# Optimization experiments

Hardware: AMD Instinct MI355X
Metric: run time of the kernel (lower is better)

Reference implementation:

```python
import jax, jax.numpy as jnp
import numpy as np
from jax import lax

NJ = 14
COL = 14
SIGMA = 1.0
RADIUS = 4  # scipy gaussian_filter: truncate=4.0 * sigma=1.0 -> radius 4


def _gauss_kernel():
    x = np.arange(-RADIUS, RADIUS + 1, dtype=np.float32)
    w = np.exp(-0.5 * x * x / (SIGMA * SIGMA))
    w /= w.sum()
    return jnp.asarray(w)


def _blur(delta):
    # separable gaussian with scipy mode='reflect' (== np.pad 'symmetric')
    B, J, H, W = delta.shape
    w = _gauss_kernel()
    p = jnp.pad(delta, ((0, 0), (0, 0), (RADIUS, RADIUS), (RADIUS, RADIUS)), mode='symmetric')
    lhs = p.reshape(B * J, 1, H + 2 * RADIUS, W + 2 * RADIUS)
    kh = w.reshape(1, 1, 2 * RADIUS + 1, 1)
    kw = w.reshape(1, 1, 1, 2 * RADIUS + 1)
    dn = ('NCHW', 'OIHW', 'NCHW')
    y = lax.conv_general_dilated(lhs, kh, (1, 1), 'VALID', dimension_numbers=dn)
    y = lax.conv_general_dilated(y, kw, (1, 1), 'VALID', dimension_numbers=dn)
    return y.reshape(B, J, H, W)


def setup_inputs() -> dict:
    key = jax.random.key(0)
    k1, k2, k3, k4 = jax.random.split(key, 4)
    B = 8192
    o = jax.random.normal(k1, (B, 2 * NJ, COL, COL), jnp.float32)
    h = jax.random.uniform(k2, (B, NJ, COL, COL), jnp.float32)
    t = jax.random.uniform(k3, (B, NJ, 2), jnp.float32)
    vis = jax.random.randint(k4, (B, NJ), 0, 2).astype(jnp.float32)
    v = jnp.repeat(vis[..., None], 2, axis=-1)  # visibility duplicated over (x,y)
    return {"o": o, "h": h, "t": t, "v": v}


def reference(o, h, t, v):
    B = h.shape[0]
    scale = 1.0 / float(COL)
    f32 = jnp.float32

    # argmax coordinate extraction from predicted heatmaps
    argmax = jnp.argmax(h.reshape(B, NJ, COL * COL), axis=-1)  # [B,Nj]
    yC = argmax // COL
    xC = argmax - yC * COL
    bidx = jnp.arange(B)[:, None]
    jidx = jnp.arange(NJ)[None, :]

    h_peak = h[bidx, jidx, yC, xC]                 # [B,Nj]
    cond = h_peak > 0.5
    ox = o[bidx, jidx, yC, xC]                     # offset channels 0..Nj-1
    oy = o[bidx, jidx + NJ, yC, xC]                # offset channels Nj..2Nj-1
    x0 = jnp.where(cond, (ox + xC.astype(f32)) * scale, 0.0)
    x1 = jnp.where(cond, (oy + yC.astype(f32)) * scale, 0.0)
    x = jnp.stack([x0, x1], axis=-1)               # [B,Nj,2]

    # per-joint gaussian target heatmap (only where visible)
    ti = t * COL
    xi = jnp.clip(ti[..., 0].astype(jnp.int32), 0, COL - 1)
    yi = jnp.clip(ti[..., 1].astype(jnp.int32), 0, COL - 1)
    visf = (v[..., 0].astype(jnp.int32) == 1).astype(f32)  # [B,Nj]
    delta = jnp.zeros((B, NJ, COL, COL), f32).at[bidx, jidx, yi, xi].set(visf)
    g = _blur(delta)
    mn = g.min(axis=(-2, -1), keepdims=True)
    mx = g.max(axis=(-2, -1), keepdims=True)
    denom = jnp.where(mx > mn, mx - mn, 1.0)
    tt = jnp.where(visf[..., None, None] > 0, (g - mn) / denom, 0.0)

    # heatmap loss; original zeroes only ROW 0 of diff for invisible joints
    diff1 = h - tt
    row0 = diff1[:, :, 0:1, :] * visf[:, :, None, None]
    diff1 = jnp.concatenate([row0, diff1[:, :, 1:, :]], axis=2)
    N1 = v.sum() / 2.0
    d1 = jnp.sum(diff1 * diff1) / N1

    # coordinate loss
    diff2 = (x - t) * v
    d2 = jnp.sum(diff2 * diff2) / N1  # N2 == N1 in the original
    return d1 + d2
```

## Files before the change

kernel.cpp:

```cpp
#include <hip/hip_runtime.h>

#define NJ    14
#define TILE  196
#define BLK   256
#define JPB   64
#define STAGE_DW (JPB * TILE)

typedef __attribute__((address_space(1))) const void g_void;
typedef __attribute__((address_space(3))) void lds_void;

__device__ __forceinline__ float gtap(int d) {
  const int d2 = d * d;
  const float e = exp2f(-0.72134752044448169f * (float)d2);
  return (d2 <= 16) ? e : 0.0f;
}

__device__ __forceinline__ float uresp(int p, int pk) {
  float s = gtap(p - pk);
  if (p <= 3)  s += gtap(p + pk + 1);
  if (p >= 10) s += gtap(27 - p - pk);
  return s;
}

__device__ __forceinline__ float wave_sum(float x) {
#pragma unroll
  for (int off = 32; off >= 1; off >>= 1) x += __shfl_xor(x, off);
  return x;
}

template<int K>
__device__ __forceinline__ void accum_part(const float4* __restrict__ hp,
    const float (&uy)[14], const float (&ux)[14],
    float& bm, int& bi, float& sh2, float& cross, float& q0)
{
  const int NI = (K == 0) ? 13 : 12;
#pragma unroll
  for (int i = 0; i < NI; ++i) {
    const int f = 4 * i + K;
    const float4 q = hp[f];
    const float qa[4] = {q.x, q.y, q.z, q.w};
#pragma unroll
    for (int c = 0; c < 4; ++c) {
      const int idx = 4 * f + c;
      const int y = idx / 14;
      const int x = idx - 14 * y;
      const float hv = qa[c];
      if (hv > bm) { bm = hv; bi = idx; }
      sh2 = fmaf(hv, hv, sh2);
      if (y == 0) q0 = fmaf(hv, hv, q0);
      cross = fmaf(hv, uy[y] * ux[x], cross);
    }
  }
}

__global__ __launch_bounds__(BLK, 3) void joint_kernel(
    const float* __restrict__ o, const float* __restrict__ h,
    const float* __restrict__ t, const float* __restrict__ v,
    float* __restrict__ part, int njoint, int nblocks)
{
  __shared__ __align__(16) float lds[STAGE_DW];

  const int tid  = threadIdx.x;
  const int lane = tid & 63;
  const int wid  = tid >> 6;
  const int jg   = blockIdx.x * JPB + lane;
  const bool valid = jg < njoint;

  const int ntile = min(JPB, njoint - blockIdx.x * JPB);
  const int n4 = ntile * 49;
  const float* gbase = h + (size_t)blockIdx.x * JPB * TILE;
#pragma unroll
  for (int i = 0; i < 13; ++i) {
    const int idx = i * BLK + tid;
    if (idx < n4) {
      __builtin_amdgcn_global_load_lds(
          (g_void*)(gbase + (size_t)idx * 4),
          (lds_void*)&lds[idx * 4],
          16, 0, 0);
    }
  }

  float uy[14], ux[14];
  float2 tv = make_float2(0.0f, 0.0f);
  int xi = 0, yi = 0;
  if (valid) {
    tv = ((const float2*)t)[jg];
    xi = min(max((int)(tv.x * 14.0f), 0), 13);
    yi = min(max((int)(tv.y * 14.0f), 0), 13);
#pragma unroll
    for (int p = 0; p < 14; ++p) { uy[p] = uresp(p, yi); ux[p] = uresp(p, xi); }
  }

  asm volatile("s_waitcnt vmcnt(0)" ::: "memory");
  __syncthreads();

  float bm = -3.0e38f; int bi = 0;
  float sh2 = 0.0f, cross = 0.0f, q0 = 0.0f;
  if (valid) {
    const float4* hp = (const float4*)&lds[lane * TILE];
    switch (wid) {
      case 0: accum_part<0>(hp, uy, ux, bm, bi, sh2, cross, q0); break;
      case 1: accum_part<1>(hp, uy, ux, bm, bi, sh2, cross, q0); break;
      case 2: accum_part<2>(hp, uy, ux, bm, bi, sh2, cross, q0); break;
      default: accum_part<3>(hp, uy, ux, bm, bi, sh2, cross, q0); break;
    }
  }

  __syncthreads();
  float* red = lds;
  red[0 * BLK + tid] = bm;
  ((int*)lds)[1 * BLK + tid] = bi;
  red[2 * BLK + tid] = sh2;
  red[3 * BLK + tid] = cross;
  red[4 * BLK + tid] = q0;
  __syncthreads();

  if (wid == 0) {
    float Bm = red[lane]; int Bi = ((int*)lds)[BLK + lane];
    float S2 = red[2 * BLK + lane], Cr = red[3 * BLK + lane], Q0 = red[4 * BLK + lane];
#pragma unroll
    for (int w = 1; w < 4; ++w) {
      const float m = red[w * 64 + lane];
      const int   i = ((int*)lds)[BLK + w * 64 + lane];
      if (m > Bm || (m == Bm && i < Bi)) { Bm = m; Bi = i; }
      S2 += red[2 * BLK + w * 64 + lane];
      Cr += red[3 * BLK + w * 64 + lane];
      Q0 += red[4 * BLK + w * 64 + lane];
    }

    float s_acc = 0.0f, n_acc = 0.0f;
    if (valid) {
      const float2 vv = ((const float2*)v)[jg];
      const bool vis = ((int)vv.x) == 1;

      float Sy2 = 0.0f, Sx2 = 0.0f;
#pragma unroll
      for (int p = 0; p < 14; ++p) {
        Sy2 = fmaf(uy[p], uy[p], Sy2);
        Sx2 = fmaf(ux[p], ux[p], Sx2);
      }
      const float maxy = 1.0f + gtap(2 * yi + 1) + gtap(27 - 2 * yi);
      const float maxx = 1.0f + gtap(2 * xi + 1) + gtap(27 - 2 * xi);
      const float inv = vis ? (1.0f / (maxy * maxx)) : 0.0f;

      float s = S2 - 2.0f * inv * Cr + inv * inv * Sy2 * Sx2;
      if (!vis) s -= Q0;

      const int b = jg / NJ;
      const int j = jg - b * NJ;
      const int yC = Bi / 14;
      const int xC = Bi - 14 * yC;
      const size_t ob = ((size_t)b * (2 * NJ) + j) * TILE + (size_t)Bi;
      const float ox = o[ob];
      const float oy = o[ob + (size_t)NJ * TILE];
      const bool cond = Bm > 0.5f;
      const float sc = 1.0f / 14.0f;
      const float px = cond ? (ox + (float)xC) * sc : 0.0f;
      const float py = cond ? (oy + (float)yC) * sc : 0.0f;
      const float d0 = (px - tv.x) * vv.x;
      const float d1 = (py - tv.y) * vv.y;
      s += d0 * d0 + d1 * d1;

      s_acc = s;
      n_acc = vv.x + vv.y;
    }

    s_acc = wave_sum(s_acc);
    n_acc = wave_sum(n_acc);
    if (lane == 0) {
      part[blockIdx.x]           = s_acc;
      part[nblocks + blockIdx.x] = n_acc;
    }
  }
}

__global__ __launch_bounds__(BLK) void finalize_kernel(
    const float* __restrict__ part, float* __restrict__ out, int nblocks)
{
  float s = 0.0f, n = 0.0f;
  for (int i = threadIdx.x; i < nblocks; i += BLK) {
    s += part[i];
    n += part[nblocks + i];
  }
  s = wave_sum(s);
  n = wave_sum(n);
  __shared__ float rs[4], rn[4];
  const int lane = threadIdx.x & 63, wid = threadIdx.x >> 6;
  if (lane == 0) { rs[wid] = s; rn[wid] = n; }
  __syncthreads();
  if (threadIdx.x == 0) {
    const float S = rs[0] + rs[1] + rs[2] + rs[3];
    const float N = rn[0] + rn[1] + rn[2] + rn[3];
    out[0] = S / (0.5f * N);
  }
}

extern "C" void kernel_launch(void* const* d_in, const int* in_sizes, int n_in,
                              void* d_out, int out_size, void* d_ws, size_t ws_size,
                              hipStream_t stream)
{
  const float* o = (const float*)d_in[0];
  const float* h = (const float*)d_in[1];
  const float* t = (const float*)d_in[2];
  const float* v = (const float*)d_in[3];
  const int njoint = in_sizes[1] / TILE;
  const int nblocks = (njoint + JPB - 1) / JPB;

  float* part = (float*)d_ws;
  joint_kernel<<<nblocks, BLK, 0, stream>>>(o, h, t, v, part, njoint, nblocks);
  finalize_kernel<<<1, BLK, 0, stream>>>(part, (float*)d_out, nblocks);
}
```

Baseline: 29.91 us.

## Assign joints per wavefront and reduce quarter-tiles with lane shuffles

Each wavefront now stages its own 16 joints into a private LDS region, so the block-wide barrier after the async loads is removed. Four adjacent lanes split one joint's tile and combine their partial max, argmax and sums with xor shuffles instead of an LDS reduction handled by wave 0. The epilogue math now runs in a quarter of the lanes of every wave rather than all lanes of one wave, and only the final per-block sum still goes through LDS. Lanes sharing a joint each compute the full blur response tables, which duplicates some setup work, and the LDS reads of the four neighbouring lanes may land in a different bank pattern.

```diff
diff --git a/kernel.cpp b/kernel.cpp
--- a/kernel.cpp
+++ b/kernel.cpp
@@ -4,7 +4,8 @@
 #define TILE  196
 #define BLK   256
 #define JPB   64
-#define STAGE_DW (JPB * TILE)
+#define TPW   16
+#define REG4  (TPW * 49)
 
 typedef __attribute__((address_space(1))) const void g_void;
 typedef __attribute__((address_space(3))) void lds_void;
@@ -28,15 +29,15 @@
   return x;
 }
 
-template<int K>
+template<int Q>
 __device__ __forceinline__ void accum_part(const float4* __restrict__ hp,
     const float (&uy)[14], const float (&ux)[14],
     float& bm, int& bi, float& sh2, float& cross, float& q0)
 {
-  const int NI = (K == 0) ? 13 : 12;
+  const int NI = (Q == 0) ? 13 : 12;
 #pragma unroll
   for (int i = 0; i < NI; ++i) {
-    const int f = 4 * i + K;
+    const int f = 4 * i + Q;
     const float4 q = hp[f];
     const float qa[4] = {q.x, q.y, q.z, q.w};
 #pragma unroll
@@ -58,25 +59,29 @@
     const float* __restrict__ t, const float* __restrict__ v,
     float* __restrict__ part, int njoint, int nblocks)
 {
-  __shared__ __align__(16) float lds[STAGE_DW];
+  __shared__ __align__(16) float lds[4 * REG4 * 4];
+  __shared__ float rs[4], rn[4];
 
   const int tid  = threadIdx.x;
   const int lane = tid & 63;
   const int wid  = tid >> 6;
-  const int jg   = blockIdx.x * JPB + lane;
+  const int tl   = lane >> 2;
+  const int qq   = lane & 3;
+  const int jg   = blockIdx.x * JPB + wid * TPW + tl;
   const bool valid = jg < njoint;
 
-  const int ntile = min(JPB, njoint - blockIdx.x * JPB);
-  const int n4 = ntile * 49;
-  const float* gbase = h + (size_t)blockIdx.x * JPB * TILE;
-#pragma unroll
-  for (int i = 0; i < 13; ++i) {
-    const int idx = i * BLK + tid;
-    if (idx < n4) {
-      __builtin_amdgcn_global_load_lds(
-          (g_void*)(gbase + (size_t)idx * 4),
-          (lds_void*)&lds[idx * 4],
-          16, 0, 0);
+  {
+    const float* gsrc = h + ((size_t)blockIdx.x * JPB + wid * TPW) * TILE;
+    float* ldst = lds + (size_t)wid * REG4 * 4;
+#pragma unroll
+    for (int i = 0; i < 13; ++i) {
+      const int f4 = i * 64 + lane;
+      if (f4 < REG4) {
+        __builtin_amdgcn_global_load_lds(
+            (g_void*)(gsrc + (size_t)f4 * 4),
+            (lds_void*)(ldst + (size_t)f4 * 4),
+            16, 0, 0);
+      }
     }
   }
 
@@ -92,13 +97,12 @@
   }
 
   asm volatile("s_waitcnt vmcnt(0)" ::: "memory");
-  __syncthreads();
 
   float bm = -3.0e38f; int bi = 0;
   float sh2 = 0.0f, cross = 0.0f, q0 = 0.0f;
   if (valid) {
-    const float4* hp = (const float4*)&lds[lane * TILE];
-    switch (wid) {
+    const float4* hp = (const float4*)(lds + ((size_t)wid * REG4 + tl * 49) * 4);
+    switch (qq) {
       case 0: accum_part<0>(hp, uy, ux, bm, bi, sh2, cross, q0); break;
       case 1: accum_part<1>(hp, uy, ux, bm, bi, sh2, cross, q0); break;
       case 2: accum_part<2>(hp, uy, ux, bm, bi, sh2, cross, q0); break;
@@ -106,71 +110,60 @@
     }
   }
 
+#pragma unroll
+  for (int off = 1; off <= 2; off <<= 1) {
+    const float om = __shfl_xor(bm, off);
+    const int   oi = __shfl_xor(bi, off);
+    if (om > bm || (om == bm && oi < bi)) { bm = om; bi = oi; }
+    sh2   += __shfl_xor(sh2, off);
+    cross += __shfl_xor(cross, off);
+    q0    += __shfl_xor(q0, off);
+  }
+
+  float s_acc = 0.0f, n_acc = 0.0f;
+  if (valid && qq == 0) {
+    const float2 vv = ((const float2*)v)[jg];
+    const bool vis = ((int)vv.x) == 1;
+
+    float Sy2 = 0.0f, Sx2 = 0.0f;
+#pragma unroll
+    for (int p = 0; p < 14; ++p) {
+      Sy2 = fmaf(uy[p], uy[p], Sy2);
+      Sx2 = fmaf(ux[p], ux[p], Sx2);
+    }
+    const float maxy = 1.0f + gtap(2 * yi + 1) + gtap(27 - 2 * yi);
+    const float maxx = 1.0f + gtap(2 * xi + 1) + gtap(27 - 2 * xi);
+    const float inv = vis ? (1.0f / (maxy * maxx)) : 0.0f;
+
+    float s = sh2 - 2.0f * inv * cross + inv * inv * Sy2 * Sx2;
+    if (!vis) s -= q0;
+
+    const int b = jg / NJ;
+    const int j = jg - b * NJ;
+    const int yC = bi / 14;
+    const int xC = bi - 14 * yC;
+    const size_t ob = ((size_t)b * (2 * NJ) + j) * TILE + (size_t)bi;
+    const float ox = o[ob];
+    const float oy = o[ob + (size_t)NJ * TILE];
+    const bool cond = bm > 0.5f;
+    const float sc = 1.0f / 14.0f;
+    const float px = cond ? (ox + (float)xC) * sc : 0.0f;
+    const float py = cond ? (oy + (float)yC) * sc : 0.0f;
+    const float d0 = (px - tv.x) * vv.x;
+    const float d1 = (py - tv.y) * vv.y;
+    s += d0 * d0 + d1 * d1;
+
+    s_acc = s;
+    n_acc = vv.x + vv.y;
+  }
+
+  s_acc = wave_sum(s_acc);
+  n_acc = wave_sum(n_acc);
+  if (lane == 0) { rs[wid] = s_acc; rn[wid] = n_acc; }
   __syncthreads();
-  float* red = lds;
-  red[0 * BLK + tid] = bm;
-  ((int*)lds)[1 * BLK + tid] = bi;
-  red[2 * BLK + tid] = sh2;
-  red[3 * BLK + tid] = cross;
-  red[4 * BLK + tid] = q0;
-  __syncthreads();
-
-  if (wid == 0) {
-    float Bm = red[lane]; int Bi = ((int*)lds)[BLK + lane];
-    float S2 = red[2 * BLK + lane], Cr = red[3 * BLK + lane], Q0 = red[4 * BLK + lane];
-#pragma unroll
-    for (int w = 1; w < 4; ++w) {
-      const float m = red[w * 64 + lane];
-      const int   i = ((int*)lds)[BLK + w * 64 + lane];
-      if (m > Bm || (m == Bm && i < Bi)) { Bm = m; Bi = i; }
-      S2 += red[2 * BLK + w * 64 + lane];
-      Cr += red[3 * BLK + w * 64 + lane];
-      Q0 += red[4 * BLK + w * 64 + lane];
-    }
-
-    float s_acc = 0.0f, n_acc = 0.0f;
-    if (valid) {
-      const float2 vv = ((const float2*)v)[jg];
-      const bool vis = ((int)vv.x) == 1;
-
-      float Sy2 = 0.0f, Sx2 = 0.0f;
-#pragma unroll
-      for (int p = 0; p < 14; ++p) {
-        Sy2 = fmaf(uy[p], uy[p], Sy2);
-        Sx2 = fmaf(ux[p], ux[p], Sx2);
-      }
-      const float maxy = 1.0f + gtap(2 * yi + 1) + gtap(27 - 2 * yi);
-      const float maxx = 1.0f + gtap(2 * xi + 1) + gtap(27 - 2 * xi);
-      const float inv = vis ? (1.0f / (maxy * maxx)) : 0.0f;
-
-      float s = S2 - 2.0f * inv * Cr + inv * inv * Sy2 * Sx2;
-      if (!vis) s -= Q0;
-
-      const int b = jg / NJ;
-      const int j = jg - b * NJ;
-      const int yC = Bi / 14;
-      const int xC = Bi - 14 * yC;
-      const size_t ob = ((size_t)b * (2 * NJ) + j) * TILE + (size_t)Bi;
-      const float ox = o[ob];
-      const float oy = o[ob + (size_t)NJ * TILE];
-      const bool cond = Bm > 0.5f;
-      const float sc = 1.0f / 14.0f;
-      const float px = cond ? (ox + (float)xC) * sc : 0.0f;
-      const float py = cond ? (oy + (float)yC) * sc : 0.0f;
-      const float d0 = (px - tv.x) * vv.x;
-      const float d1 = (py - tv.y) * vv.y;
-      s += d0 * d0 + d1 * d1;
-
-      s_acc = s;
-      n_acc = vv.x + vv.y;
-    }
-
-    s_acc = wave_sum(s_acc);
-    n_acc = wave_sum(n_acc);
-    if (lane == 0) {
-      part[blockIdx.x]           = s_acc;
-      part[nblocks + blockIdx.x] = n_acc;
-    }
+  if (tid == 0) {
+    part[blockIdx.x]           = rs[0] + rs[1] + rs[2] + rs[3];
+    part[nblocks + blockIdx.x] = rn[0] + rn[1] + rn[2] + rn[3];
   }
 }
 
```

Result: slower. 39.12 us (+30.8%).

## Halve joints per block and split each joint across eight half-wave parts

Applied to the files above, without the earlier changes.

Each block now handles 32 joints instead of 64. Each wave's two halves process different float4 slices of the same joint, so work is split eight ways and combined first with a cross-half shuffle, then through LDS. The smaller LDS footprint allows a higher occupancy hint, and the finalize kernel uses 1024 threads to sum the doubled number of partials. Bounds checks are removed, which assumes the joint count is a multiple of 32.

```diff
diff --git a/kernel.cpp b/kernel.cpp
--- a/kernel.cpp
+++ b/kernel.cpp
@@ -3,8 +3,8 @@
 #define NJ    14
 #define TILE  196
 #define BLK   256
-#define JPB   64
-#define STAGE_DW (JPB * TILE)
+#define JPB   32
+#define N4    (JPB * 49)
 
 typedef __attribute__((address_space(1))) const void g_void;
 typedef __attribute__((address_space(3))) void lds_void;
@@ -28,15 +28,15 @@
   return x;
 }
 
-template<int K>
+template<int P>
 __device__ __forceinline__ void accum_part(const float4* __restrict__ hp,
     const float (&uy)[14], const float (&ux)[14],
     float& bm, int& bi, float& sh2, float& cross, float& q0)
 {
-  const int NI = (K == 0) ? 13 : 12;
+  const int NI = (P == 0) ? 7 : 6;
 #pragma unroll
   for (int i = 0; i < NI; ++i) {
-    const int f = 4 * i + K;
+    const int f = 8 * i + P;
     const float4 q = hp[f];
     const float qa[4] = {q.x, q.y, q.z, q.w};
 #pragma unroll
@@ -53,26 +53,24 @@
   }
 }
 
-__global__ __launch_bounds__(BLK, 3) void joint_kernel(
+__global__ __launch_bounds__(BLK, 6) void joint_kernel(
     const float* __restrict__ o, const float* __restrict__ h,
     const float* __restrict__ t, const float* __restrict__ v,
     float* __restrict__ part, int njoint, int nblocks)
 {
-  __shared__ __align__(16) float lds[STAGE_DW];
+  __shared__ __align__(16) float lds[N4 * 4];
 
   const int tid  = threadIdx.x;
   const int lane = tid & 63;
   const int wid  = tid >> 6;
-  const int jg   = blockIdx.x * JPB + lane;
-  const bool valid = jg < njoint;
-
-  const int ntile = min(JPB, njoint - blockIdx.x * JPB);
-  const int n4 = ntile * 49;
+  const int tl   = tid & 31;
+  const int jg   = blockIdx.x * JPB + tl;
+
   const float* gbase = h + (size_t)blockIdx.x * JPB * TILE;
 #pragma unroll
-  for (int i = 0; i < 13; ++i) {
+  for (int i = 0; i < 7; ++i) {
     const int idx = i * BLK + tid;
-    if (idx < n4) {
+    if (idx < N4) {
       __builtin_amdgcn_global_load_lds(
           (g_void*)(gbase + (size_t)idx * 4),
           (lds_void*)&lds[idx * 4],
@@ -81,55 +79,68 @@
   }
 
   float uy[14], ux[14];
-  float2 tv = make_float2(0.0f, 0.0f);
-  int xi = 0, yi = 0;
-  if (valid) {
-    tv = ((const float2*)t)[jg];
-    xi = min(max((int)(tv.x * 14.0f), 0), 13);
-    yi = min(max((int)(tv.y * 14.0f), 0), 13);
-#pragma unroll
-    for (int p = 0; p < 14; ++p) { uy[p] = uresp(p, yi); ux[p] = uresp(p, xi); }
-  }
+  const float2 tv = ((const float2*)t)[jg];
+  const int xi = min(max((int)(tv.x * 14.0f), 0), 13);
+  const int yi = min(max((int)(tv.y * 14.0f), 0), 13);
+#pragma unroll
+  for (int p = 0; p < 14; ++p) { uy[p] = uresp(p, yi); ux[p] = uresp(p, xi); }
 
   asm volatile("s_waitcnt vmcnt(0)" ::: "memory");
   __syncthreads();
 
   float bm = -3.0e38f; int bi = 0;
   float sh2 = 0.0f, cross = 0.0f, q0 = 0.0f;
-  if (valid) {
-    const float4* hp = (const float4*)&lds[lane * TILE];
+  {
+    const float4* hp = (const float4*)&lds[tl * TILE];
     switch (wid) {
-      case 0: accum_part<0>(hp, uy, ux, bm, bi, sh2, cross, q0); break;
-      case 1: accum_part<1>(hp, uy, ux, bm, bi, sh2, cross, q0); break;
-      case 2: accum_part<2>(hp, uy, ux, bm, bi, sh2, cross, q0); break;
-      default: accum_part<3>(hp, uy, ux, bm, bi, sh2, cross, q0); break;
-    }
-  }
-
-  __syncthreads();
-  float* red = lds;
-  red[0 * BLK + tid] = bm;
-  ((int*)lds)[1 * BLK + tid] = bi;
-  red[2 * BLK + tid] = sh2;
-  red[3 * BLK + tid] = cross;
-  red[4 * BLK + tid] = q0;
-  __syncthreads();
-
+      case 0:  if (lane < 32) accum_part<0>(hp, uy, ux, bm, bi, sh2, cross, q0);
+               else           accum_part<1>(hp, uy, ux, bm, bi, sh2, cross, q0); break;
+      case 1:  if (lane < 32) accum_part<2>(hp, uy, ux, bm, bi, sh2, cross, q0);
+               else           accum_part<3>(hp, uy, ux, bm, bi, sh2, cross, q0); break;
+      case 2:  if (lane < 32) accum_part<4>(hp, uy, ux, bm, bi, sh2, cross, q0);
+               else           accum_part<5>(hp, uy, ux, bm, bi, sh2, cross, q0); break;
+      default: if (lane < 32) accum_part<6>(hp, uy, ux, bm, bi, sh2, cross, q0);
+               else           accum_part<7>(hp, uy, ux, bm, bi, sh2, cross, q0); break;
+    }
+  }
+
+  {
+    const float om = __shfl_xor(bm, 32);
+    const int   oi = __shfl_xor(bi, 32);
+    if (om > bm || (om == bm && oi < bi)) { bm = om; bi = oi; }
+    sh2   += __shfl_xor(sh2, 32);
+    cross += __shfl_xor(cross, 32);
+    q0    += __shfl_xor(q0, 32);
+  }
+
+  __syncthreads();
+  if (lane < 32) {
+    lds[(0 * 4 + wid) * 32 + tl] = bm;
+    ((int*)lds)[(1 * 4 + wid) * 32 + tl] = bi;
+    lds[(2 * 4 + wid) * 32 + tl] = sh2;
+    lds[(3 * 4 + wid) * 32 + tl] = cross;
+    lds[(4 * 4 + wid) * 32 + tl] = q0;
+  }
+  __syncthreads();
+
+  float s_acc = 0.0f, n_acc = 0.0f;
   if (wid == 0) {
-    float Bm = red[lane]; int Bi = ((int*)lds)[BLK + lane];
-    float S2 = red[2 * BLK + lane], Cr = red[3 * BLK + lane], Q0 = red[4 * BLK + lane];
-#pragma unroll
-    for (int w = 1; w < 4; ++w) {
-      const float m = red[w * 64 + lane];
-      const int   i = ((int*)lds)[BLK + w * 64 + lane];
-      if (m > Bm || (m == Bm && i < Bi)) { Bm = m; Bi = i; }
-      S2 += red[2 * BLK + w * 64 + lane];
-      Cr += red[3 * BLK + w * 64 + lane];
-      Q0 += red[4 * BLK + w * 64 + lane];
-    }
-
-    float s_acc = 0.0f, n_acc = 0.0f;
-    if (valid) {
+    if (lane < 32) {
+      float Bm = lds[0 * 128 + lane];
+      int   Bi = ((int*)lds)[1 * 128 + lane];
+      float S2 = lds[2 * 128 + lane];
+      float Cr = lds[3 * 128 + lane];
+      float Q0 = lds[4 * 128 + lane];
+#pragma unroll
+      for (int w = 1; w < 4; ++w) {
+        const float m = lds[0 * 128 + w * 32 + lane];
+        const int   i = ((int*)lds)[1 * 128 + w * 32 + lane];
+        if (m > Bm || (m == Bm && i < Bi)) { Bm = m; Bi = i; }
+        S2 += lds[2 * 128 + w * 32 + lane];
+        Cr += lds[3 * 128 + w * 32 + lane];
+        Q0 += lds[4 * 128 + w * 32 + lane];
+      }
+
       const float2 vv = ((const float2*)v)[jg];
       const bool vis = ((int)vv.x) == 1;
 
@@ -164,7 +175,6 @@
       s_acc = s;
       n_acc = vv.x + vv.y;
     }
-
     s_acc = wave_sum(s_acc);
     n_acc = wave_sum(n_acc);
     if (lane == 0) {
@@ -174,23 +184,25 @@
   }
 }
 
-__global__ __launch_bounds__(BLK) void finalize_kernel(
+#define FBLK 1024
+__global__ __launch_bounds__(FBLK) void finalize_kernel(
     const float* __restrict__ part, float* __restrict__ out, int nblocks)
 {
   float s = 0.0f, n = 0.0f;
-  for (int i = threadIdx.x; i < nblocks; i += BLK) {
+  for (int i = threadIdx.x; i < nblocks; i += FBLK) {
     s += part[i];
     n += part[nblocks + i];
   }
   s = wave_sum(s);
   n = wave_sum(n);
-  __shared__ float rs[4], rn[4];
+  __shared__ float rs[16], rn[16];
   const int lane = threadIdx.x & 63, wid = threadIdx.x >> 6;
   if (lane == 0) { rs[wid] = s; rn[wid] = n; }
   __syncthreads();
   if (threadIdx.x == 0) {
-    const float S = rs[0] + rs[1] + rs[2] + rs[3];
-    const float N = rn[0] + rn[1] + rn[2] + rn[3];
+    float S = 0.0f, N = 0.0f;
+#pragma unroll
+    for (int i = 0; i < 16; ++i) { S += rs[i]; N += rn[i]; }
     out[0] = S / (0.5f * N);
   }
 }
@@ -204,9 +216,9 @@
   const float* t = (const float*)d_in[2];
   const float* v = (const float*)d_in[3];
   const int njoint = in_sizes[1] / TILE;
-  const int nblocks = (njoint + JPB - 1) / JPB;
+  const int nblocks = njoint / JPB;
 
   float* part = (float*)d_ws;
   joint_kernel<<<nblocks, BLK, 0, stream>>>(o, h, t, v, part, njoint, nblocks);
-  finalize_kernel<<<1, BLK, 0, stream>>>(part, (float*)d_out, nblocks);
-}
+  finalize_kernel<<<1, FBLK, 0, stream>>>(part, (float*)d_out, nblocks);
+}
```

Measured after the change: 50.03 us. 1.67x slower.
